# Optimization experiments

Measured on AMD Instinct MI355X. Metric: run time of the kernel, lower is better.

## Reference

```python
import jax, jax.numpy as jnp
import numpy as np

IN, OUT, HID = 256, 256, 512
BATCH, T = 16, 4096


def setup_inputs() -> dict:
    key = jax.random.key(0)
    ks = jax.random.split(key, 10)
    # nu/theta init as in the original module (r_min=0, r_max=1)
    u1 = jax.random.uniform(ks[0], (HID,))
    nu = -0.5 * jnp.log(u1)  # uniform in (0,1) -> nu > 0
    nu_log = jnp.log(nu)
    theta = (jnp.pi / 10.0) * jax.random.uniform(ks[1], (HID,))
    theta_log = jnp.log(theta)
    # glorot-uniform style scales
    sB = float(np.sqrt(6.0 / (HID + IN)))
    sC = float(np.sqrt(6.0 / (OUT + HID)))
    sD = float(np.sqrt(6.0 / (OUT + IN)))
    B_re = jax.random.uniform(ks[2], (HID, IN), minval=-sB, maxval=sB)
    B_im = jax.random.uniform(ks[3], (HID, IN), minval=-sB, maxval=sB)
    C_re = jax.random.uniform(ks[4], (OUT, HID), minval=-sC, maxval=sC)
    C_im = jax.random.uniform(ks[5], (OUT, HID), minval=-sC, maxval=sC)
    D = jax.random.uniform(ks[6], (OUT, IN), minval=-sD, maxval=sD)
    bh_re = jnp.zeros((HID,), jnp.float32)
    bh_im = jnp.zeros((HID,), jnp.float32)
    bias_output = jnp.zeros((OUT,), jnp.float32)
    X = jax.random.normal(ks[7], (BATCH, T, IN), dtype=jnp.float32)
    return {
        "X": X, "nu_log": nu_log, "theta_log": theta_log,
        "B_re": B_re, "B_im": B_im, "C_re": C_re, "C_im": C_im,
        "D": D, "bh_re": bh_re, "bh_im": bh_im, "bias_output": bias_output,
    }


def reference(X, nu_log, theta_log, B_re, B_im, C_re, C_im, D, bh_re, bh_im, bias_output):
    # lambda = exp(-exp(nu_log) + i*exp(theta_log));  |lambda| = exp(-exp(nu_log))
    mag = jnp.exp(-jnp.exp(nu_log))                       # [H], real
    lam = mag * jnp.exp(1j * jnp.exp(theta_log))          # [H], complex64
    gamma = jnp.sqrt(1.0 - mag * mag)                     # [H], real
    B = B_re + 1j * B_im                                  # [H, I]
    C = C_re + 1j * C_im                                  # [O, H]
    bias_h = bh_re + 1j * bh_im                           # [H]
    # input drive precomputed for all timesteps: gamma * (B @ x_t) + bias_hidden
    Bu = jnp.einsum("bti,hi->bth", X.astype(jnp.complex64), B)  # [B,T,H]
    drive = gamma.astype(jnp.complex64) * Bu + bias_h           # [B,T,H]

    def step(h, d_t):  # h: [B,H] complex, d_t: [B,H] complex
        h = lam * h + d_t
        return h, h

    h0 = jnp.zeros((X.shape[0], lam.shape[0]), jnp.complex64)
    _, H = jax.lax.scan(step, h0, jnp.swapaxes(drive, 0, 1))  # H: [T,B,H]
    H = jnp.swapaxes(H, 0, 1)                                 # [B,T,H]
    Y = (jnp.real(jnp.einsum("bth,oh->bto", H, C))
         + jnp.einsum("bti,oi->bto", X, D)
         + bias_output)
    return Y
```

## Files before the change

### kernel.cpp

```cpp
#include <hip/hip_runtime.h>
#include <hip/hip_bf16.h>


#define TT     4096
#define BATCHN 16
#define MM     (BATCHN * TT)
#define LCH    64
#define NCH    (TT / LCH)

typedef unsigned short u16;
typedef short bf16x8 __attribute__((ext_vector_type(8)));
typedef float f32x4 __attribute__((ext_vector_type(4)));

__device__ __forceinline__ u16 f2bf(float f) {
  union { __hip_bfloat16 b; u16 u; } cv;
  cv.b = __float2bfloat16(f);
  return cv.u;
}
__device__ __forceinline__ float bf2f(u16 u) {
  union { u16 u; __hip_bfloat16 b; } cv;
  cv.u = u;
  return __bfloat162float(cv.b);
}

__global__ void k_params(const float* __restrict__ nu_log,
                         const float* __restrict__ theta_log,
                         float* __restrict__ P) {
  int h = threadIdx.x;
  if (h >= 512) return;
  double nu  = exp((double)nu_log[h]);
  double th  = exp((double)theta_log[h]);
  double mag = exp(-nu);
  double g   = sqrt(fmax(0.0, 1.0 - mag * mag));
  double magL = exp(-(double)LCH * nu);
  double aL   = (double)LCH * th;
  P[h]        = (float)(mag * cos(th));
  P[512 + h]  = (float)(mag * sin(th));
  P[1024 + h] = (float)g;
  P[1536 + h] = (float)(magL * cos(aL));
  P[2048 + h] = (float)(magL * sin(aL));
}

__global__ void k_prep_w(const float* __restrict__ Bre, const float* __restrict__ Bim,
                         const float* __restrict__ Cre, const float* __restrict__ Cim,
                         const float* __restrict__ D, u16* __restrict__ Bcat,
                         u16* __restrict__ Ccat) {
  const int NB = 1024 * 256;
  const int NC = 256 * 1280;
  for (int idx = blockIdx.x * blockDim.x + threadIdx.x; idx < NB + NC;
       idx += gridDim.x * blockDim.x) {
    if (idx < NB) {
      int row = idx >> 8, col = idx & 255;
      float v = (row < 512) ? Bre[row * 256 + col] : Bim[(row - 512) * 256 + col];
      Bcat[idx] = f2bf(v);
    } else {
      int j = idx - NB;
      int o = j / 1280, k = j % 1280;
      float v;
      if (k < 1024) {
        int q = k >> 9, kk = k & 511;
        int h = q * 256 + (kk & 255);
        v = (kk < 256) ? Cre[o * 512 + h] : -Cim[o * 512 + h];
      } else {
        v = D[o * 256 + (k - 1024)];
      }
      Ccat[j] = f2bf(v);
    }
  }
}

__global__ __launch_bounds__(256) void k_prep_x(const float* __restrict__ X,
                                                u16* __restrict__ Xb) {
  int idx = blockIdx.x * 256 + threadIdx.x;
  const float4* s = (const float4*)X + (size_t)idx * 2;
  float4 a = s[0], b = s[1];
  u16 o[8] = {f2bf(a.x), f2bf(a.y), f2bf(a.z), f2bf(a.w),
              f2bf(b.x), f2bf(b.y), f2bf(b.z), f2bf(b.w)};
  *(int4*)(Xb + (size_t)idx * 8) = *(const int4*)o;
}

__global__ __launch_bounds__(256) void k_gemm1(
    const u16* __restrict__ Xb, const u16* __restrict__ Bcat,
    const float* __restrict__ P, const float* __restrict__ bhr,
    const float* __restrict__ bhi, u16* __restrict__ Hbuf) {
  __shared__ __align__(16) char smem[2 * 128 * 64 * 2];
  char* sA = smem;
  char* sB = smem + 128 * 64 * 2;
  const int tid = threadIdx.x;
  const int lane = tid & 63;
  const int wid = tid >> 6;
  const int wr = wid >> 1, wc = wid & 1;
  const int mb = blockIdx.x * 128;
  const int nb = blockIdx.y * 128;

  f32x4 acc[4][4];
#pragma unroll
  for (int r = 0; r < 4; ++r)
#pragma unroll
    for (int c = 0; c < 4; ++c) acc[r][c] = (f32x4)0.f;

  for (int kt = 0; kt < 4; ++kt) {
    const int k0 = kt * 64;
    __syncthreads();
#pragma unroll
    for (int i = 0; i < 4; ++i) {
      int s = i * 256 + tid;
      int row = s >> 3, slot = s & 7;
      int4 va = *(const int4*)(Xb + (size_t)(mb + row) * 256 + k0 + slot * 8);
      int4 vb = *(const int4*)(Bcat + (size_t)(nb + row) * 256 + k0 + slot * 8);
      int soff = row * 128 + ((slot ^ (row & 7)) << 4);
      *(int4*)(sA + soff) = va;
      *(int4*)(sB + soff) = vb;
    }
    __syncthreads();
#pragma unroll
    for (int kk = 0; kk < 2; ++kk) {
      bf16x8 af[4], bfr[4];
#pragma unroll
      for (int r = 0; r < 4; ++r) {
        int row = wr * 64 + r * 16 + (lane & 15);
        int slot = (kk * 4 + (lane >> 4)) ^ (row & 7);
        af[r] = *(const bf16x8*)(sA + row * 128 + slot * 16);
      }
#pragma unroll
      for (int c = 0; c < 4; ++c) {
        int row = wc * 64 + c * 16 + (lane & 15);
        int slot = (kk * 4 + (lane >> 4)) ^ (row & 7);
        bfr[c] = *(const bf16x8*)(sB + row * 128 + slot * 16);
      }
#pragma unroll
      for (int r = 0; r < 4; ++r)
#pragma unroll
        for (int c = 0; c < 4; ++c)
          acc[r][c] = __builtin_amdgcn_mfma_f32_16x16x32_bf16(af[r], bfr[c],
                                                              acc[r][c], 0, 0, 0);
    }
  }
  const int rbase = (lane >> 4) * 4;
  const int cbase = lane & 15;
#pragma unroll
  for (int r = 0; r < 4; ++r)
#pragma unroll
    for (int c = 0; c < 4; ++c) {
      int col = nb + wc * 64 + c * 16 + cbase;
      int h = col & 511;
      float g = P[1024 + h];
      float bias = (col < 512) ? bhr[h] : bhi[h];
#pragma unroll
      for (int q = 0; q < 4; ++q) {
        int row = mb + wr * 64 + r * 16 + rbase + q;
        Hbuf[(size_t)row * 1024 + col] = f2bf(fmaf(acc[r][c][q], g, bias));
      }
    }
}

__global__ __launch_bounds__(512) void k_scanF(
    const float* __restrict__ P, const u16* __restrict__ Hbuf,
    float* __restrict__ finr, float* __restrict__ fini) {
  const int h = threadIdx.x;
  const int b = blockIdx.x, c = blockIdx.y;
  const float lr = P[h], li = P[512 + h];
  float hr = 0.f, hi = 0.f;
  size_t base = ((size_t)b * TT + (size_t)c * LCH) * 1024 + h;
#pragma unroll 8
  for (int j = 0; j < LCH; ++j) {
    float dr = bf2f(Hbuf[base]);
    float di = bf2f(Hbuf[base + 512]);
    float nr = fmaf(lr, hr, fmaf(-li, hi, dr));
    float ni = fmaf(lr, hi, fmaf(li, hr, di));
    hr = nr; hi = ni;
    base += 1024;
  }
  size_t f = ((size_t)b * NCH + c) * 512 + h;
  finr[f] = hr; fini[f] = hi;
}

__global__ __launch_bounds__(512) void k_carry(
    const float* __restrict__ P, const float* __restrict__ finr,
    const float* __restrict__ fini, float* __restrict__ carr,
    float* __restrict__ cari) {
  const int h = threadIdx.x;
  const int b = blockIdx.x;
  const float Lr = P[1536 + h], Li = P[2048 + h];
  float cr = 0.f, ci = 0.f;
  for (int c = 0; c < NCH; ++c) {
    size_t idx = ((size_t)b * NCH + c) * 512 + h;
    carr[idx] = cr; cari[idx] = ci;
    float fr = finr[idx], fi = fini[idx];
    float nr = fmaf(Lr, cr, fmaf(-Li, ci, fr));
    float ni = fmaf(Lr, ci, fmaf(Li, cr, fi));
    cr = nr; ci = ni;
  }
}

__global__ __launch_bounds__(256) void k_fused2(
    const float* __restrict__ P, const u16* __restrict__ Hbuf,
    const u16* __restrict__ Xb, const u16* __restrict__ Ccat,
    const float* __restrict__ carr, const float* __restrict__ cari,
    const float* __restrict__ bo, float* __restrict__ Y) {
  __shared__ __align__(16) char Hs[64 * 1024];
  const int tid = threadIdx.x;
  const int lane = tid & 63;
  const int w = tid >> 6;
  const int c = blockIdx.x;
  const int b = blockIdx.y;
  const int row0 = b * TT + c * LCH;

  f32x4 acc[4][4];
#pragma unroll
  for (int m = 0; m < 4; ++m)
#pragma unroll
    for (int n = 0; n < 4; ++n) acc[m][n] = (f32x4)0.f;

#pragma unroll
  for (int q = 0; q < 2; ++q) {
    const int h = q * 256 + tid;
    const float lr = P[h], li = P[512 + h];
    size_t cidx = ((size_t)b * NCH + c) * 512 + h;
    float hr = carr[cidx], hi = cari[cidx];
    size_t base = (size_t)row0 * 1024 + h;
    __syncthreads();
#pragma unroll 8
    for (int j = 0; j < LCH; ++j) {
      float dr = bf2f(Hbuf[base]);
      float di = bf2f(Hbuf[base + 512]);
      float nr = fmaf(lr, hr, fmaf(-li, hi, dr));
      float ni = fmaf(lr, hi, fmaf(li, hr, di));
      hr = nr; hi = ni;
      int sre = ((tid >> 3) ^ (j & 7)) * 16 + (tid & 7) * 2;
      int sim = (((256 + tid) >> 3) ^ (j & 7)) * 16 + (tid & 7) * 2;
      *(u16*)(Hs + j * 1024 + sre) = f2bf(nr);
      *(u16*)(Hs + j * 1024 + sim) = f2bf(ni);
      base += 1024;
    }
    __syncthreads();
#pragma unroll 4
    for (int ks = 0; ks < 16; ++ks) {
      bf16x8 af[4], bfr[4];
#pragma unroll
      for (int m = 0; m < 4; ++m) {
        int row = m * 16 + (lane & 15);
        int slot = (ks * 4 + (lane >> 4)) ^ (row & 7);
        af[m] = *(const bf16x8*)(Hs + row * 1024 + slot * 16);
      }
#pragma unroll
      for (int n = 0; n < 4; ++n) {
        int col = w * 64 + n * 16 + (lane & 15);
        bfr[n] = *(const bf16x8*)(Ccat + (size_t)col * 1280 + q * 512 +
                                  ks * 32 + (lane >> 4) * 8);
      }
#pragma unroll
      for (int m = 0; m < 4; ++m)
#pragma unroll
        for (int n = 0; n < 4; ++n)
          acc[m][n] = __builtin_amdgcn_mfma_f32_16x16x32_bf16(af[m], bfr[n],
                                                              acc[m][n], 0, 0, 0);
    }
  }

  __syncthreads();
#pragma unroll
  for (int i = 0; i < 8; ++i) {
    int p = i * 256 + tid;
    int row = p >> 5, slot = p & 31;
    int4 v = *(const int4*)(Xb + (size_t)(row0 + row) * 256 +
                            ((slot ^ (row & 7)) * 8));
    *(int4*)(Hs + row * 512 + slot * 16) = v;
  }
  __syncthreads();
#pragma unroll 2
  for (int ks = 0; ks < 8; ++ks) {
    bf16x8 af[4], bfr[4];
#pragma unroll
    for (int m = 0; m < 4; ++m) {
      int row = m * 16 + (lane & 15);
      int slot = (ks * 4 + (lane >> 4)) ^ (row & 7);
      af[m] = *(const bf16x8*)(Hs + row * 512 + slot * 16);
    }
#pragma unroll
    for (int n = 0; n < 4; ++n) {
      int col = w * 64 + n * 16 + (lane & 15);
      bfr[n] = *(const bf16x8*)(Ccat + (size_t)col * 1280 + 1024 +
                                ks * 32 + (lane >> 4) * 8);
    }
#pragma unroll
    for (int m = 0; m < 4; ++m)
#pragma unroll
      for (int n = 0; n < 4; ++n)
        acc[m][n] = __builtin_amdgcn_mfma_f32_16x16x32_bf16(af[m], bfr[n],
                                                            acc[m][n], 0, 0, 0);
  }

  const int rb = (lane >> 4) * 4;
  const int cb = lane & 15;
#pragma unroll
  for (int m = 0; m < 4; ++m)
#pragma unroll
    for (int n = 0; n < 4; ++n) {
      int col = w * 64 + n * 16 + cb;
      float bias = bo[col];
#pragma unroll
      for (int qq = 0; qq < 4; ++qq) {
        int row = row0 + m * 16 + rb + qq;
        Y[(size_t)row * 256 + col] = acc[m][n][qq] + bias;
      }
    }
}

extern "C" void kernel_launch(void* const* d_in, const int* in_sizes, int n_in,
                              void* d_out, int out_size, void* d_ws, size_t ws_size,
                              hipStream_t stream) {
  const float* X        = (const float*)d_in[0];
  const float* nu_log   = (const float*)d_in[1];
  const float* theta_lg = (const float*)d_in[2];
  const float* Bre      = (const float*)d_in[3];
  const float* Bim      = (const float*)d_in[4];
  const float* Cre      = (const float*)d_in[5];
  const float* Cim      = (const float*)d_in[6];
  const float* D        = (const float*)d_in[7];
  const float* bhr      = (const float*)d_in[8];
  const float* bhi      = (const float*)d_in[9];
  const float* bo       = (const float*)d_in[10];
  float* Y = (float*)d_out;
  char* ws = (char*)d_ws;

  size_t off = 0;
  float* P = (float*)(ws + off);            off += 2560 * 4;
  off = (off + 255) & ~(size_t)255;
  u16* Hbuf = (u16*)(ws + off);             off += (size_t)MM * 1024 * 2;
  u16* Xb   = (u16*)(ws + off);             off += (size_t)MM * 256 * 2;
  u16* Bcat = (u16*)(ws + off);             off += 1024 * 256 * 2;
  u16* Ccat = (u16*)(ws + off);             off += 256 * 1280 * 2;
  float* finr = (float*)(ws + off);         off += (size_t)BATCHN * NCH * 512 * 4;
  float* fini = (float*)(ws + off);         off += (size_t)BATCHN * NCH * 512 * 4;
  float* carr = (float*)(ws + off);         off += (size_t)BATCHN * NCH * 512 * 4;
  float* cari = (float*)(ws + off);         off += (size_t)BATCHN * NCH * 512 * 4;
  if (ws_size < off) return;

  k_params<<<1, 512, 0, stream>>>(nu_log, theta_lg, P);
  k_prep_w<<<512, 256, 0, stream>>>(Bre, Bim, Cre, Cim, D, Bcat, Ccat);
  k_prep_x<<<MM * 256 / (256 * 8), 256, 0, stream>>>(X, Xb);
  k_gemm1<<<dim3(MM / 128, 8), 256, 0, stream>>>(Xb, Bcat, P, bhr, bhi, Hbuf);
  k_scanF<<<dim3(BATCHN, NCH), 512, 0, stream>>>(P, Hbuf, finr, fini);
  k_carry<<<BATCHN, 512, 0, stream>>>(P, finr, fini, carr, cari);
  k_fused2<<<dim3(NCH, BATCHN), 256, 0, stream>>>(P, Hbuf, Xb, Ccat, carr, cari,
                                                  bo, Y);
}
```

Before: 324.2 us.

## Fuse chunk-final scan into GEMM1, interleave re/im, and restructure fused2 scan

Re and im hidden channels are interleaved so each packed u32 holds one complex value. The per-chunk final-state scan moves into k_gemm1's epilogue through an LDS tile, which removes the separate k_scanF pass over Hbuf. GEMM1 tile loads switch to direct global-to-LDS loads. k_fused2 now has each thread own one complex channel, uses a two-step (lambda^2) recurrence to shorten the dependency chain, prefetches the second half's drive and X into registers while MFMAs run, and requests two blocks per CU. The cost is heavy register use (two 64-entry u32 arrays) with a risk of spills, plus extra LDS traffic in GEMM1.

```diff
diff --git a/kernel.cpp b/kernel.cpp
--- a/kernel.cpp
+++ b/kernel.cpp
@@ -9,6 +9,7 @@
 #define NCH    (TT / LCH)
 
 typedef unsigned short u16;
+typedef unsigned int u32;
 typedef short bf16x8 __attribute__((ext_vector_type(8)));
 typedef float f32x4 __attribute__((ext_vector_type(4)));
 
@@ -21,6 +22,12 @@
   union { u16 u; __hip_bfloat16 b; } cv;
   cv.u = u;
   return __bfloat162float(cv.b);
+}
+
+typedef __attribute__((address_space(3))) char lds_char;
+typedef __attribute__((address_space(1))) const char gbl_char;
+__device__ __forceinline__ void gload16(const void* g, void* l) {
+  __builtin_amdgcn_global_load_lds((gbl_char*)g, (lds_char*)l, 16, 0, 0);
 }
 
 __global__ void k_params(const float* __restrict__ nu_log,
@@ -34,11 +41,14 @@
   double g   = sqrt(fmax(0.0, 1.0 - mag * mag));
   double magL = exp(-(double)LCH * nu);
   double aL   = (double)LCH * th;
+  double mag2 = exp(-2.0 * nu);
   P[h]        = (float)(mag * cos(th));
   P[512 + h]  = (float)(mag * sin(th));
   P[1024 + h] = (float)g;
   P[1536 + h] = (float)(magL * cos(aL));
   P[2048 + h] = (float)(magL * sin(aL));
+  P[2560 + h] = (float)(mag2 * cos(2.0 * th));
+  P[3072 + h] = (float)(mag2 * sin(2.0 * th));
 }
 
 __global__ void k_prep_w(const float* __restrict__ Bre, const float* __restrict__ Bim,
@@ -51,16 +61,16 @@
        idx += gridDim.x * blockDim.x) {
     if (idx < NB) {
       int row = idx >> 8, col = idx & 255;
-      float v = (row < 512) ? Bre[row * 256 + col] : Bim[(row - 512) * 256 + col];
+      int ch = row >> 1;
+      float v = (row & 1) ? Bim[ch * 256 + col] : Bre[ch * 256 + col];
       Bcat[idx] = f2bf(v);
     } else {
       int j = idx - NB;
       int o = j / 1280, k = j % 1280;
       float v;
       if (k < 1024) {
-        int q = k >> 9, kk = k & 511;
-        int h = q * 256 + (kk & 255);
-        v = (kk < 256) ? Cre[o * 512 + h] : -Cim[o * 512 + h];
+        int ch = k >> 1;
+        v = (k & 1) ? -Cim[o * 512 + ch] : Cre[o * 512 + ch];
       } else {
         v = D[o * 256 + (k - 1024)];
       }
@@ -82,10 +92,12 @@
 __global__ __launch_bounds__(256) void k_gemm1(
     const u16* __restrict__ Xb, const u16* __restrict__ Bcat,
     const float* __restrict__ P, const float* __restrict__ bhr,
-    const float* __restrict__ bhi, u16* __restrict__ Hbuf) {
-  __shared__ __align__(16) char smem[2 * 128 * 64 * 2];
+    const float* __restrict__ bhi, u16* __restrict__ Hbuf,
+    float* __restrict__ finr, float* __restrict__ fini) {
+  __shared__ __align__(16) char smem[33280];
   char* sA = smem;
-  char* sB = smem + 128 * 64 * 2;
+  char* sB = smem + 16384;
+  u32* sF = (u32*)smem;
   const int tid = threadIdx.x;
   const int lane = tid & 63;
   const int wid = tid >> 6;
@@ -106,11 +118,9 @@
     for (int i = 0; i < 4; ++i) {
       int s = i * 256 + tid;
       int row = s >> 3, slot = s & 7;
-      int4 va = *(const int4*)(Xb + (size_t)(mb + row) * 256 + k0 + slot * 8);
-      int4 vb = *(const int4*)(Bcat + (size_t)(nb + row) * 256 + k0 + slot * 8);
-      int soff = row * 128 + ((slot ^ (row & 7)) << 4);
-      *(int4*)(sA + soff) = va;
-      *(int4*)(sB + soff) = vb;
+      int swz = slot ^ (row & 7);
+      gload16(Xb + (size_t)(mb + row) * 256 + k0 + swz * 8, sA + s * 16);
+      gload16(Bcat + (size_t)(nb + row) * 256 + k0 + swz * 8, sB + s * 16);
     }
     __syncthreads();
 #pragma unroll
@@ -136,43 +146,50 @@
                                                               acc[r][c], 0, 0, 0);
     }
   }
+  __syncthreads();
+
   const int rbase = (lane >> 4) * 4;
   const int cbase = lane & 15;
 #pragma unroll
   for (int r = 0; r < 4; ++r)
 #pragma unroll
     for (int c = 0; c < 4; ++c) {
-      int col = nb + wc * 64 + c * 16 + cbase;
-      int h = col & 511;
-      float g = P[1024 + h];
-      float bias = (col < 512) ? bhr[h] : bhi[h];
+      int col_l = wc * 64 + c * 16 + cbase;
+      int col = nb + col_l;
+      int ch = col >> 1;
+      float g = P[1024 + ch];
+      float bias = (col & 1) ? bhi[ch] : bhr[ch];
 #pragma unroll
       for (int q = 0; q < 4; ++q) {
-        int row = mb + wr * 64 + r * 16 + rbase + q;
-        Hbuf[(size_t)row * 1024 + col] = f2bf(fmaf(acc[r][c][q], g, bias));
-      }
-    }
-}
-
-__global__ __launch_bounds__(512) void k_scanF(
-    const float* __restrict__ P, const u16* __restrict__ Hbuf,
-    float* __restrict__ finr, float* __restrict__ fini) {
-  const int h = threadIdx.x;
-  const int b = blockIdx.x, c = blockIdx.y;
-  const float lr = P[h], li = P[512 + h];
-  float hr = 0.f, hi = 0.f;
-  size_t base = ((size_t)b * TT + (size_t)c * LCH) * 1024 + h;
+        int row_l = wr * 64 + r * 16 + rbase + q;
+        int row = mb + row_l;
+        u16 v = f2bf(fmaf(acc[r][c][q], g, bias));
+        Hbuf[(size_t)row * 1024 + col] = v;
+        char* p = (char*)&sF[row_l * 65 + (col_l >> 1)];
+        *(u16*)(p + (col_l & 1) * 2) = v;
+      }
+    }
+  __syncthreads();
+
+  if (tid < 128) {
+    int ch_l = tid & 63, half = tid >> 6;
+    int ch = blockIdx.y * 64 + ch_l;
+    float lr = P[ch], li = P[512 + ch];
+    float hr = 0.f, hi = 0.f;
 #pragma unroll 8
-  for (int j = 0; j < LCH; ++j) {
-    float dr = bf2f(Hbuf[base]);
-    float di = bf2f(Hbuf[base + 512]);
-    float nr = fmaf(lr, hr, fmaf(-li, hi, dr));
-    float ni = fmaf(lr, hi, fmaf(li, hr, di));
-    hr = nr; hi = ni;
-    base += 1024;
-  }
-  size_t f = ((size_t)b * NCH + c) * 512 + h;
-  finr[f] = hr; fini[f] = hi;
+    for (int j = 0; j < LCH; ++j) {
+      u32 pk = sF[(half * 64 + j) * 65 + ch_l];
+      float dr = bf2f((u16)(pk & 0xffff));
+      float di = bf2f((u16)(pk >> 16));
+      float nr = fmaf(lr, hr, fmaf(-li, hi, dr));
+      float ni = fmaf(lr, hi, fmaf(li, hr, di));
+      hr = nr; hi = ni;
+    }
+    int b = mb >> 12;
+    int chunk = ((mb & 4095) >> 6) + half;
+    size_t f = ((size_t)b * NCH + chunk) * 512 + ch;
+    finr[f] = hr; fini[f] = hi;
+  }
 }
 
 __global__ __launch_bounds__(512) void k_carry(
@@ -193,7 +210,48 @@
   }
 }
 
-__global__ __launch_bounds__(256) void k_fused2(
+#define CHAIN_PHASE(DBUF, CR, CI, LR, LI, LR2, LI2)                         \
+  {                                                                         \
+    float ur = (CR), ui = (CI);                                             \
+    _Pragma("unroll") for (int k = 0; k < 32; ++k) {                        \
+      u32 p0 = DBUF[2 * k], p1 = DBUF[2 * k + 1];                           \
+      float der = bf2f((u16)(p0 & 0xffff)), dei = bf2f((u16)(p0 >> 16));    \
+      float dor = bf2f((u16)(p1 & 0xffff)), doi = bf2f((u16)(p1 >> 16));    \
+      float er = fmaf((LR), der, fmaf(-(LI), dei, dor));                    \
+      float ei = fmaf((LR), dei, fmaf((LI), der, doi));                     \
+      float h0r = fmaf((LR), ur, fmaf(-(LI), ui, der));                     \
+      float h0i = fmaf((LR), ui, fmaf((LI), ur, dei));                      \
+      float nur = fmaf((LR2), ur, fmaf(-(LI2), ui, er));                    \
+      float nui = fmaf((LR2), ui, fmaf((LI2), ur, ei));                     \
+      int j0 = 2 * k, j1 = 2 * k + 1;                                       \
+      int s0 = ((tid >> 2) ^ (j0 & 7)) * 16 + (tid & 3) * 4;                \
+      int s1 = ((tid >> 2) ^ (j1 & 7)) * 16 + (tid & 3) * 4;                \
+      *(u32*)(Hs + j0 * 1024 + s0) = (u32)f2bf(h0r) | ((u32)f2bf(h0i) << 16); \
+      *(u32*)(Hs + j1 * 1024 + s1) = (u32)f2bf(nur) | ((u32)f2bf(nui) << 16); \
+      ur = nur; ui = nui;                                                   \
+    }                                                                       \
+  }
+
+#define MFMA_PHASE(QOFF)                                                    \
+  _Pragma("unroll 4") for (int ks = 0; ks < 16; ++ks) {                     \
+    bf16x8 af[4], bfr[4];                                                   \
+    _Pragma("unroll") for (int m = 0; m < 4; ++m) {                         \
+      int row = m * 16 + (lane & 15);                                       \
+      int slot = (ks * 4 + (lane >> 4)) ^ (row & 7);                        \
+      af[m] = *(const bf16x8*)(Hs + row * 1024 + slot * 16);                \
+    }                                                                       \
+    _Pragma("unroll") for (int n = 0; n < 4; ++n) {                         \
+      int col = w * 64 + n * 16 + (lane & 15);                              \
+      bfr[n] = *(const bf16x8*)(Ccat + (size_t)col * 1280 + (QOFF) +        \
+                                ks * 32 + (lane >> 4) * 8);                 \
+    }                                                                       \
+    _Pragma("unroll") for (int m = 0; m < 4; ++m)                           \
+      _Pragma("unroll") for (int n = 0; n < 4; ++n)                         \
+        acc[m][n] = __builtin_amdgcn_mfma_f32_16x16x32_bf16(af[m], bfr[n],  \
+                                                            acc[m][n], 0, 0, 0); \
+  }
+
+__global__ __launch_bounds__(256, 2) void k_fused2(
     const float* __restrict__ P, const u16* __restrict__ Hbuf,
     const u16* __restrict__ Xb, const u16* __restrict__ Ccat,
     const float* __restrict__ carr, const float* __restrict__ cari,
@@ -212,60 +270,53 @@
 #pragma unroll
     for (int n = 0; n < 4; ++n) acc[m][n] = (f32x4)0.f;
 
-#pragma unroll
-  for (int q = 0; q < 2; ++q) {
-    const int h = q * 256 + tid;
-    const float lr = P[h], li = P[512 + h];
-    size_t cidx = ((size_t)b * NCH + c) * 512 + h;
-    float hr = carr[cidx], hi = cari[cidx];
-    size_t base = (size_t)row0 * 1024 + h;
-    __syncthreads();
-#pragma unroll 8
-    for (int j = 0; j < LCH; ++j) {
-      float dr = bf2f(Hbuf[base]);
-      float di = bf2f(Hbuf[base + 512]);
-      float nr = fmaf(lr, hr, fmaf(-li, hi, dr));
-      float ni = fmaf(lr, hi, fmaf(li, hr, di));
-      hr = nr; hi = ni;
-      int sre = ((tid >> 3) ^ (j & 7)) * 16 + (tid & 7) * 2;
-      int sim = (((256 + tid) >> 3) ^ (j & 7)) * 16 + (tid & 7) * 2;
-      *(u16*)(Hs + j * 1024 + sre) = f2bf(nr);
-      *(u16*)(Hs + j * 1024 + sim) = f2bf(ni);
-      base += 1024;
-    }
-    __syncthreads();
-#pragma unroll 4
-    for (int ks = 0; ks < 16; ++ks) {
-      bf16x8 af[4], bfr[4];
-#pragma unroll
-      for (int m = 0; m < 4; ++m) {
-        int row = m * 16 + (lane & 15);
-        int slot = (ks * 4 + (lane >> 4)) ^ (row & 7);
-        af[m] = *(const bf16x8*)(Hs + row * 1024 + slot * 16);
-      }
-#pragma unroll
-      for (int n = 0; n < 4; ++n) {
-        int col = w * 64 + n * 16 + (lane & 15);
-        bfr[n] = *(const bf16x8*)(Ccat + (size_t)col * 1280 + q * 512 +
-                                  ks * 32 + (lane >> 4) * 8);
-      }
-#pragma unroll
-      for (int m = 0; m < 4; ++m)
-#pragma unroll
-        for (int n = 0; n < 4; ++n)
-          acc[m][n] = __builtin_amdgcn_mfma_f32_16x16x32_bf16(af[m], bfr[n],
-                                                              acc[m][n], 0, 0, 0);
-    }
-  }
-
-  __syncthreads();
+  const u32* H32 = (const u32*)Hbuf;
+  const size_t cidx = ((size_t)b * NCH + c) * 512 + tid;
+  const size_t base0 = (size_t)row0 * 512 + tid;
+
+  u32 d0[64];
+#pragma unroll
+  for (int j = 0; j < 64; ++j) d0[j] = H32[base0 + (size_t)j * 512];
+  float car0r = carr[cidx], car0i = cari[cidx];
+  {
+    const float lr = P[tid], li = P[512 + tid];
+    const float lr2 = P[2560 + tid], li2 = P[3072 + tid];
+    CHAIN_PHASE(d0, car0r, car0i, lr, li, lr2, li2)
+  }
+
+  u32 d1[64];
+#pragma unroll
+  for (int j = 0; j < 64; ++j) d1[j] = H32[base0 + 256 + (size_t)j * 512];
+  float car1r = carr[cidx + 256], car1i = cari[cidx + 256];
+
+  __syncthreads();
+  MFMA_PHASE(0)
+  __syncthreads();
+
+  {
+    const float lr = P[256 + tid], li = P[768 + tid];
+    const float lr2 = P[2816 + tid], li2 = P[3328 + tid];
+    CHAIN_PHASE(d1, car1r, car1i, lr, li, lr2, li2)
+  }
+
+  int4 xstg[8];
 #pragma unroll
   for (int i = 0; i < 8; ++i) {
     int p = i * 256 + tid;
     int row = p >> 5, slot = p & 31;
-    int4 v = *(const int4*)(Xb + (size_t)(row0 + row) * 256 +
-                            ((slot ^ (row & 7)) * 8));
-    *(int4*)(Hs + row * 512 + slot * 16) = v;
+    xstg[i] = *(const int4*)(Xb + (size_t)(row0 + row) * 256 +
+                             ((slot ^ (row & 7)) * 8));
+  }
+
+  __syncthreads();
+  MFMA_PHASE(512)
+  __syncthreads();
+
+#pragma unroll
+  for (int i = 0; i < 8; ++i) {
+    int p = i * 256 + tid;
+    int row = p >> 5, slot = p & 31;
+    *(int4*)(Hs + row * 512 + slot * 16) = xstg[i];
   }
   __syncthreads();
 #pragma unroll 2
@@ -325,7 +376,7 @@
   char* ws = (char*)d_ws;
 
   size_t off = 0;
-  float* P = (float*)(ws + off);            off += 2560 * 4;
+  float* P = (float*)(ws + off);            off += 4096 * 4;
   off = (off + 255) & ~(size_t)255;
   u16* Hbuf = (u16*)(ws + off);             off += (size_t)MM * 1024 * 2;
   u16* Xb   = (u16*)(ws + off);             off += (size_t)MM * 256 * 2;
@@ -340,8 +391,8 @@
   k_params<<<1, 512, 0, stream>>>(nu_log, theta_lg, P);
   k_prep_w<<<512, 256, 0, stream>>>(Bre, Bim, Cre, Cim, D, Bcat, Ccat);
   k_prep_x<<<MM * 256 / (256 * 8), 256, 0, stream>>>(X, Xb);
-  k_gemm1<<<dim3(MM / 128, 8), 256, 0, stream>>>(Xb, Bcat, P, bhr, bhi, Hbuf);
-  k_scanF<<<dim3(BATCHN, NCH), 512, 0, stream>>>(P, Hbuf, finr, fini);
+  k_gemm1<<<dim3(MM / 128, 8), 256, 0, stream>>>(Xb, Bcat, P, bhr, bhi, Hbuf,
+                                                 finr, fini);
   k_carry<<<BATCHN, 512, 0, stream>>>(P, finr, fini, carr, cari);
   k_fused2<<<dim3(NCH, BATCHN), 256, 0, stream>>>(P, Hbuf, Xb, Ccat, carr, cari,
                                                   bo, Y);
```

New measurement: 332.2 us. 1.02x slower.
